# Kernel optimization log

Measured on AMD Instinct MI355X. Metric: run time of the kernel, lower is better.

Reference implementation:

```python
import jax, jax.numpy as jnp
import numpy as np

B, H, LK, D = 8, 16, 4096, 128


def setup_inputs() -> dict:
    key = jax.random.key(0)
    ks = jax.random.split(key, 9)
    s = 1.0 / np.sqrt(D)
    return {
        "Q": jax.random.normal(ks[0], (B, H, 1, D), dtype=jnp.float32),
        "K": jax.random.normal(ks[1], (B, H, LK, D), dtype=jnp.float32),
        "V": jax.random.normal(ks[2], (B, H, LK, D), dtype=jnp.float32),
        "mask": jax.random.randint(ks[3], (B, H, 1, LK), 0, 2, dtype=jnp.int32),
        "scale": 1,  # accepted but unused by the original forward
        "W_pre": jax.random.normal(ks[4], (D, D), dtype=jnp.float32) * s,
        "b_pre": jax.random.normal(ks[5], (D,), dtype=jnp.float32) * s,
        "W_q": jax.random.normal(ks[6], (D, D), dtype=jnp.float32) * s,
        "W_v": jax.random.normal(ks[7], (D, 1), dtype=jnp.float32) * s,
    }


def reference(Q, K, V, mask, scale, W_pre, b_pre, W_q, W_v):
    # precompute = linear_pre(K): [B,H,LK,D]
    pre = jnp.einsum("bhkd,de->bhke", K, W_pre) + b_pre
    # targetT = linear_q(Q): [B,H,1,D], broadcast-added over keys
    tq = jnp.einsum("bhqd,de->bhqe", Q, W_q)
    tmp = jnp.tanh(pre + tq)  # [B,H,LK,D]
    # energy = linear_v(tmp) reshaped to [B,H,1,LK]
    energy = jnp.einsum("bhkd,d->bhk", tmp, W_v[:, 0])[:, :, None, :]
    m = mask.astype(energy.dtype)
    energy = energy * (1.0 - m) + m * (-1e6)
    score = jax.nn.softmax(energy, axis=-1)  # [B,H,1,LK]
    context = jnp.matmul(score, V)  # [B,H,1,D]
    return (context, score, pre)
```

## Files before the change

kernel.cpp:

```cpp
#include <hip/hip_runtime.h>
#include <hip/hip_bf16.h>
#include <math.h>

#define B_   8
#define H_   16
#define BH_  (B_*H_)
#define LK_  4096
#define D_   128

#define SEG   16
#define KSEG  (LK_/SEG)

typedef __attribute__((ext_vector_type(8))) short bf16x8;
typedef __attribute__((ext_vector_type(4))) float f32x4;
typedef __attribute__((ext_vector_type(4))) unsigned int u32x4;

__device__ __forceinline__ float fast_tanh(float x) {
    float ax = fabsf(x);
    float e  = __expf(2.0f * ax);
    float r  = 1.0f - __fdividef(2.0f, e + 1.0f);
    return copysignf(r, x);
}

__device__ __forceinline__ unsigned int cvtpk(float lo, float hi) {
    unsigned int r;
    asm("v_cvt_pk_bf16_f32 %0, %1, %2" : "=v"(r) : "v"(lo), "v"(hi));
    return r;
}

__device__ __forceinline__ unsigned short cvt_hi(float x) {
    __hip_bfloat16 bh = __float2bfloat16(x);
    return __builtin_bit_cast(unsigned short, bh);
}

__device__ __forceinline__ void cvt8(const float4 a, const float4 b, bf16x8& h, bf16x8& l) {
    unsigned int h0 = cvtpk(a.x, a.y);
    unsigned int h1 = cvtpk(a.z, a.w);
    unsigned int h2 = cvtpk(b.x, b.y);
    unsigned int h3 = cvtpk(b.z, b.w);
    float l0 = a.x - __uint_as_float(h0 << 16);
    float l1 = a.y - __uint_as_float(h0 & 0xFFFF0000u);
    float l2 = a.z - __uint_as_float(h1 << 16);
    float l3 = a.w - __uint_as_float(h1 & 0xFFFF0000u);
    float l4 = b.x - __uint_as_float(h2 << 16);
    float l5 = b.y - __uint_as_float(h2 & 0xFFFF0000u);
    float l6 = b.z - __uint_as_float(h3 << 16);
    float l7 = b.w - __uint_as_float(h3 & 0xFFFF0000u);
    u32x4 hv = {h0, h1, h2, h3};
    u32x4 lv = {cvtpk(l0, l1), cvtpk(l2, l3), cvtpk(l4, l5), cvtpk(l6, l7)};
    h = __builtin_bit_cast(bf16x8, hv);
    l = __builtin_bit_cast(bf16x8, lv);
}

__global__ void pack_kernel(const float* __restrict__ Wpre,
                            unsigned short* __restrict__ Whi) {
    int idx  = blockIdx.x * 256 + threadIdx.x;
    int j    = idx & 7;
    int lane = (idx >> 3) & 63;
    int nt   = (idx >> 9) & 7;
    int ks   = idx >> 12;
    int k    = ks * 32 + (lane >> 4) * 8 + j;
    int n    = nt * 16 + (lane & 15);
    Whi[idx] = cvt_hi(Wpre[k * D_ + n]);
}

__global__ void tq_kernel(const float* __restrict__ Q,
                          const float* __restrict__ Wq,
                          float* __restrict__ tq) {
    int bh = blockIdx.x;
    int e  = threadIdx.x;
    const float* q = Q + bh * D_;
    float acc = 0.0f;
#pragma unroll 8
    for (int d = 0; d < D_; ++d)
        acc = fmaf(q[d], Wq[d * D_ + e], acc);
    tq[bh * D_ + e] = acc;
}

__global__ void __launch_bounds__(256, 3)
main_kernel(const float* __restrict__ K,
            const unsigned short* __restrict__ Whi,
            const float* __restrict__ bpre,
            const float* __restrict__ Wv,
            const float* __restrict__ tqg,
            float* __restrict__ pre_out,
            float* __restrict__ ep0,
            float* __restrict__ ep1) {
    const int t    = threadIdx.x;
    const int lane = t & 63;
    const int wv_  = t >> 6;
    const int kg   = wv_ & 1;
    const int eh   = wv_ >> 1;
    const int l15  = lane & 15;
    const int lg   = lane >> 4;
    const int bh   = blockIdx.y;
    const int kblk = blockIdx.x * 256;

    __shared__ unsigned short Wlds[16384];
    {
        const u32x4* src = (const u32x4*)Whi;
        u32x4* dst = (u32x4*)Wlds;
#pragma unroll
        for (int i = 0; i < 8; ++i)
            dst[i * 256 + t] = src[i * 256 + t];
    }
    __syncthreads();

    const float* Kw = K + ((size_t)bh * LK_ + kblk + kg * 32 + l15) * D_ + lg * 8;
    float* epo = (eh == 0) ? ep0 : ep1;
    const unsigned short* wb = Wlds + (size_t)(eh * 4) * 512 + (size_t)lane * 8;

    float4 rw[3][2][2];
#pragma unroll
    for (int s = 0; s < 2; ++s) {
#pragma unroll
        for (int kt = 0; kt < 2; ++kt) {
            const float* p = Kw + ((size_t)kt * 16) * D_ + s * 32;
            rw[s][kt][0] = *(const float4*)p;
            rw[s][kt][1] = *(const float4*)(p + 4);
        }
    }

#pragma unroll
    for (int it = 0; it < 4; ++it) {
        f32x4 acc[2][4];
#pragma unroll
        for (int kt = 0; kt < 2; ++kt)
#pragma unroll
            for (int et = 0; et < 4; ++et)
                acc[kt][et] = (f32x4){0.f, 0.f, 0.f, 0.f};

#pragma unroll
        for (int ks = 0; ks < 4; ++ks) {
            const int s = it * 4 + ks;
            if (s + 2 < 16) {
                const int s2  = s + 2;
                const int it2 = s2 >> 2, ks2 = s2 & 3, b2 = s2 % 3;
#pragma unroll
                for (int kt = 0; kt < 2; ++kt) {
                    const float* p = Kw + ((size_t)it2 * 64 + kt * 16) * D_ + ks2 * 32;
                    rw[b2][kt][0] = *(const float4*)p;
                    rw[b2][kt][1] = *(const float4*)(p + 4);
                }
            }
            bf16x8 wf[4];
#pragma unroll
            for (int et = 0; et < 4; ++et)
                wf[et] = *(const bf16x8*)(wb + ((size_t)ks * 8 + et) * 512);
            const int cb = s % 3;
            bf16x8 kh[2], kl[2];
            cvt8(rw[cb][0][0], rw[cb][0][1], kh[0], kl[0]);
            cvt8(rw[cb][1][0], rw[cb][1][1], kh[1], kl[1]);
#pragma unroll
            for (int kt = 0; kt < 2; ++kt)
#pragma unroll
                for (int et = 0; et < 4; ++et) {
                    acc[kt][et] = __builtin_amdgcn_mfma_f32_16x16x32_bf16(wf[et], kh[kt], acc[kt][et], 0, 0, 0);
                    acc[kt][et] = __builtin_amdgcn_mfma_f32_16x16x32_bf16(wf[et], kl[kt], acc[kt][et], 0, 0, 0);
                }
        }

        const int kb = kblk + it * 64 + kg * 32;
        float ep[2] = {0.0f, 0.0f};
#pragma unroll
        for (int et = 0; et < 4; ++et) {
            const int e0 = eh * 64 + et * 16 + lg * 4;
            const float4 bp = *(const float4*)(bpre + e0);
            const float4 tq = *(const float4*)(tqg + bh * D_ + e0);
            const float4 wv = *(const float4*)(Wv + e0);
#pragma unroll
            for (int kt = 0; kt < 2; ++kt) {
                f32x4 a = acc[kt][et];
                f32x4 v;
                v[0] = a[0] + bp.x;
                v[1] = a[1] + bp.y;
                v[2] = a[2] + bp.z;
                v[3] = a[3] + bp.w;
                float* pb = pre_out + ((size_t)bh * LK_ + kb + kt * 16 + l15) * D_ + e0;
                __builtin_nontemporal_store(v, (f32x4*)pb);
                ep[kt] = fmaf(fast_tanh(v[0] + tq.x), wv.x, ep[kt]);
                ep[kt] = fmaf(fast_tanh(v[1] + tq.y), wv.y, ep[kt]);
                ep[kt] = fmaf(fast_tanh(v[2] + tq.z), wv.z, ep[kt]);
                ep[kt] = fmaf(fast_tanh(v[3] + tq.w), wv.w, ep[kt]);
            }
        }
#pragma unroll
        for (int kt = 0; kt < 2; ++kt) {
            float v = ep[kt];
            v += __shfl_xor(v, 16, 64);
            v += __shfl_xor(v, 32, 64);
            if (lg == 0)
                epo[(size_t)bh * LK_ + kb + kt * 16 + l15] = v;
        }
    }
}

__global__ void ml_kernel(const float* __restrict__ ep0,
                          const float* __restrict__ ep1,
                          const int* __restrict__ mask,
                          float* __restrict__ ml) {
    const int bh = blockIdx.x;
    const int t  = threadIdx.x;
    const float* e0 = ep0 + (size_t)bh * LK_;
    const float* e1 = ep1 + (size_t)bh * LK_;
    const int*   m  = mask + (size_t)bh * LK_;

    float mx = -1e30f;
    for (int k = t; k < LK_; k += 256) {
        float v = m[k] ? -1.0e6f : (e0[k] + e1[k]);
        mx = fmaxf(mx, v);
    }
#pragma unroll
    for (int off = 32; off > 0; off >>= 1)
        mx = fmaxf(mx, __shfl_xor(mx, off, 64));
    __shared__ float wmax[4];
    if ((t & 63) == 0) wmax[t >> 6] = mx;
    __syncthreads();
    mx = fmaxf(fmaxf(wmax[0], wmax[1]), fmaxf(wmax[2], wmax[3]));

    float sum = 0.0f;
    for (int k = t; k < LK_; k += 256) {
        float v = m[k] ? -1.0e6f : (e0[k] + e1[k]);
        sum += __expf(v - mx);
    }
#pragma unroll
    for (int off = 32; off > 0; off >>= 1)
        sum += __shfl_xor(sum, off, 64);
    __shared__ float wsum[4];
    if ((t & 63) == 0) wsum[t >> 6] = sum;
    __syncthreads();
    if (t == 0) {
        ml[bh * 2]     = mx;
        ml[bh * 2 + 1] = wsum[0] + wsum[1] + wsum[2] + wsum[3];
    }
}

__global__ void score_ctx_kernel(const float* __restrict__ ep1,
                                 const int* __restrict__ mask,
                                 const float* __restrict__ V,
                                 const float* __restrict__ ml,
                                 float* __restrict__ score_out,
                                 float* __restrict__ part) {
    const int seg = blockIdx.x;
    const int bh  = blockIdx.y;
    const int t   = threadIdx.x;
    const int k0  = seg * KSEG;

    __shared__ float sc[KSEG];
    __shared__ float pl[8][136];

    const float mx  = ml[bh * 2];
    const float inv = 1.0f / ml[bh * 2 + 1];

    {
        const size_t gi = (size_t)bh * LK_ + k0 + t;
        float v = mask[gi] ? -1.0e6f : (score_out[gi] + ep1[gi]);
        float s = __expf(v - mx) * inv;
        sc[t] = s;
        score_out[gi] = s;
    }
    __syncthreads();

    const int d4 = t & 31;
    const int g  = t >> 5;
    const float* Vb = V + ((size_t)bh * LK_ + k0) * D_ + d4 * 4;
    float4 a = make_float4(0.f, 0.f, 0.f, 0.f);
#pragma unroll 4
    for (int kk = g; kk < KSEG; kk += 8) {
        float4 vv = *(const float4*)(Vb + (size_t)kk * D_);
        float s = sc[kk];
        a.x = fmaf(s, vv.x, a.x);
        a.y = fmaf(s, vv.y, a.y);
        a.z = fmaf(s, vv.z, a.z);
        a.w = fmaf(s, vv.w, a.w);
    }
    *(float4*)&pl[g][d4 * 4] = a;
    __syncthreads();

    if (t < 128) {
        float s = 0.0f;
#pragma unroll
        for (int gg = 0; gg < 8; ++gg)
            s += pl[gg][t];
        part[((size_t)bh * SEG + seg) * D_ + t] = s;
    }
}

__global__ void combine_kernel(const float* __restrict__ part,
                               float* __restrict__ ctx) {
    const int bh = blockIdx.x;
    const int d  = threadIdx.x;
    float s = 0.0f;
#pragma unroll
    for (int g = 0; g < SEG; ++g)
        s += part[((size_t)bh * SEG + g) * D_ + d];
    ctx[bh * D_ + d] = s;
}

extern "C" void kernel_launch(void* const* d_in, const int* in_sizes, int n_in,
                              void* d_out, int out_size, void* d_ws, size_t ws_size,
                              hipStream_t stream) {
    const float* Q    = (const float*)d_in[0];
    const float* K    = (const float*)d_in[1];
    const float* V    = (const float*)d_in[2];
    const int*   mask = (const int*)  d_in[3];
    const float* Wpre = (const float*)d_in[5];
    const float* bpre = (const float*)d_in[6];
    const float* Wq   = (const float*)d_in[7];
    const float* Wv   = (const float*)d_in[8];

    float* out   = (float*)d_out;
    float* ctx   = out;
    float* score = out + (size_t)BH_ * D_;
    float* pre   = score + (size_t)BH_ * LK_;

    float* w    = (float*)d_ws;
    float* tq   = w;
    float* ml   = tq + (size_t)BH_ * D_;
    float* part = ml + 2 * BH_;
    unsigned short* Whi = (unsigned short*)(part + (size_t)BH_ * SEG * D_);
    float* ep1  = (float*)(Whi + 16384);

    hipLaunchKernelGGL(pack_kernel, dim3(64), dim3(256), 0, stream, Wpre, Whi);
    hipLaunchKernelGGL(tq_kernel, dim3(BH_), dim3(D_), 0, stream, Q, Wq, tq);
    hipLaunchKernelGGL(main_kernel, dim3(LK_ / 256, BH_), dim3(256), 0, stream,
                       K, Whi, bpre, Wv, tq, pre, score, ep1);
    hipLaunchKernelGGL(ml_kernel, dim3(BH_), dim3(256), 0, stream, score, ep1, mask, ml);
    hipLaunchKernelGGL(score_ctx_kernel, dim3(SEG, BH_), dim3(256), 0, stream,
                       ep1, mask, V, ml, score, part);
    hipLaunchKernelGGL(combine_kernel, dim3(BH_), dim3(D_), 0, stream, part, ctx);
}
```

Measured before the change: 236.3 us.

## Stage K tiles via global_load_lds double buffering and keep W fragments in registers

Replaces direct per-thread register loads of K with asynchronous global-to-LDS loads into a double-buffered shared tile, processing 32 keys per step with a barrier after each step. The W_pre bf16 fragments are now loaded once from global memory into registers instead of being staged through LDS. The intent is to overlap K fetches with MFMA work and cut register pressure from the triple-buffered K registers. In exchange it adds a block-wide barrier every step, and the s_waitcnt vmcnt(0) also waits on the nontemporal pre_out stores, which may serialize memory traffic.

```diff
diff --git a/kernel.cpp b/kernel.cpp
--- a/kernel.cpp
+++ b/kernel.cpp
@@ -33,23 +33,30 @@
     return __builtin_bit_cast(unsigned short, bh);
 }
 
-__device__ __forceinline__ void cvt8(const float4 a, const float4 b, bf16x8& h, bf16x8& l) {
-    unsigned int h0 = cvtpk(a.x, a.y);
-    unsigned int h1 = cvtpk(a.z, a.w);
-    unsigned int h2 = cvtpk(b.x, b.y);
-    unsigned int h3 = cvtpk(b.z, b.w);
-    float l0 = a.x - __uint_as_float(h0 << 16);
-    float l1 = a.y - __uint_as_float(h0 & 0xFFFF0000u);
-    float l2 = a.z - __uint_as_float(h1 << 16);
-    float l3 = a.w - __uint_as_float(h1 & 0xFFFF0000u);
-    float l4 = b.x - __uint_as_float(h2 << 16);
-    float l5 = b.y - __uint_as_float(h2 & 0xFFFF0000u);
-    float l6 = b.z - __uint_as_float(h3 << 16);
-    float l7 = b.w - __uint_as_float(h3 & 0xFFFF0000u);
+__device__ __forceinline__ void cvt8v(const f32x4 a, const f32x4 b, bf16x8& h, bf16x8& l) {
+    unsigned int h0 = cvtpk(a[0], a[1]);
+    unsigned int h1 = cvtpk(a[2], a[3]);
+    unsigned int h2 = cvtpk(b[0], b[1]);
+    unsigned int h3 = cvtpk(b[2], b[3]);
+    float l0 = a[0] - __uint_as_float(h0 << 16);
+    float l1 = a[1] - __uint_as_float(h0 & 0xFFFF0000u);
+    float l2 = a[2] - __uint_as_float(h1 << 16);
+    float l3 = a[3] - __uint_as_float(h1 & 0xFFFF0000u);
+    float l4 = b[0] - __uint_as_float(h2 << 16);
+    float l5 = b[1] - __uint_as_float(h2 & 0xFFFF0000u);
+    float l6 = b[2] - __uint_as_float(h3 << 16);
+    float l7 = b[3] - __uint_as_float(h3 & 0xFFFF0000u);
     u32x4 hv = {h0, h1, h2, h3};
     u32x4 lv = {cvtpk(l0, l1), cvtpk(l2, l3), cvtpk(l4, l5), cvtpk(l6, l7)};
     h = __builtin_bit_cast(bf16x8, hv);
     l = __builtin_bit_cast(bf16x8, lv);
+}
+
+__device__ __forceinline__ void gld_lds16(const void* g, void* l) {
+    __builtin_amdgcn_global_load_lds(
+        (const __attribute__((address_space(1))) unsigned int*)g,
+        (__attribute__((address_space(3))) unsigned int*)l,
+        16, 0, 0);
 }
 
 __global__ void pack_kernel(const float* __restrict__ Wpre,
@@ -96,102 +103,83 @@
     const int bh   = blockIdx.y;
     const int kblk = blockIdx.x * 256;
 
-    __shared__ unsigned short Wlds[16384];
-    {
-        const u32x4* src = (const u32x4*)Whi;
-        u32x4* dst = (u32x4*)Wlds;
-#pragma unroll
-        for (int i = 0; i < 8; ++i)
-            dst[i * 256 + t] = src[i * 256 + t];
-    }
-    __syncthreads();
-
-    const float* Kw = K + ((size_t)bh * LK_ + kblk + kg * 32 + l15) * D_ + lg * 8;
-    float* epo = (eh == 0) ? ep0 : ep1;
-    const unsigned short* wb = Wlds + (size_t)(eh * 4) * 512 + (size_t)lane * 8;
-
-    float4 rw[3][2][2];
-#pragma unroll
-    for (int s = 0; s < 2; ++s) {
-#pragma unroll
-        for (int kt = 0; kt < 2; ++kt) {
-            const float* p = Kw + ((size_t)kt * 16) * D_ + s * 32;
-            rw[s][kt][0] = *(const float4*)p;
-            rw[s][kt][1] = *(const float4*)(p + 4);
+    __shared__ float Klds[2][4096];
+
+    const float* Kbh = K + (size_t)bh * LK_ * D_;
+
+    bf16x8 wf[4][4];
+#pragma unroll
+    for (int ks = 0; ks < 4; ++ks)
+#pragma unroll
+        for (int et = 0; et < 4; ++et)
+            wf[ks][et] = *(const bf16x8*)(Whi + (((size_t)ks * 8 + eh * 4 + et) * 64 + lane) * 8);
+
+    auto stageK = [&](int s, int buf) {
+#pragma unroll
+        for (int i = 0; i < 4; ++i) {
+            const int g4  = wv_ * 4 + i;
+            const int kg2 = g4 >> 3, ks2 = (g4 >> 1) & 3, h2 = g4 & 1;
+            const int row = kblk + s * 32 + kg2 * 16 + l15;
+            const int col = lg * 8 + ks2 * 32 + h2 * 4;
+            gld_lds16(Kbh + (size_t)row * D_ + col, &Klds[buf][g4 * 256]);
         }
-    }
-
-#pragma unroll
-    for (int it = 0; it < 4; ++it) {
-        f32x4 acc[2][4];
-#pragma unroll
-        for (int kt = 0; kt < 2; ++kt)
-#pragma unroll
-            for (int et = 0; et < 4; ++et)
-                acc[kt][et] = (f32x4){0.f, 0.f, 0.f, 0.f};
+    };
+
+    stageK(0, 0);
+    asm volatile("s_waitcnt vmcnt(0)\n\ts_barrier" ::: "memory");
+
+#pragma unroll
+    for (int s = 0; s < 8; ++s) {
+        if (s < 7) stageK(s + 1, (s + 1) & 1);
+
+        const float* kb = Klds[s & 1];
+        f32x4 acc[4];
+#pragma unroll
+        for (int et = 0; et < 4; ++et)
+            acc[et] = (f32x4){0.f, 0.f, 0.f, 0.f};
 
 #pragma unroll
         for (int ks = 0; ks < 4; ++ks) {
-            const int s = it * 4 + ks;
-            if (s + 2 < 16) {
-                const int s2  = s + 2;
-                const int it2 = s2 >> 2, ks2 = s2 & 3, b2 = s2 % 3;
-#pragma unroll
-                for (int kt = 0; kt < 2; ++kt) {
-                    const float* p = Kw + ((size_t)it2 * 64 + kt * 16) * D_ + ks2 * 32;
-                    rw[b2][kt][0] = *(const float4*)p;
-                    rw[b2][kt][1] = *(const float4*)(p + 4);
-                }
+            const int gbase = ((kg * 4 + ks) * 2) * 256 + lane * 4;
+            f32x4 p0 = *(const f32x4*)(kb + gbase);
+            f32x4 p1 = *(const f32x4*)(kb + gbase + 256);
+            bf16x8 kh, kl;
+            cvt8v(p0, p1, kh, kl);
+#pragma unroll
+            for (int et = 0; et < 4; ++et) {
+                acc[et] = __builtin_amdgcn_mfma_f32_16x16x32_bf16(wf[ks][et], kh, acc[et], 0, 0, 0);
+                acc[et] = __builtin_amdgcn_mfma_f32_16x16x32_bf16(wf[ks][et], kl, acc[et], 0, 0, 0);
             }
-            bf16x8 wf[4];
-#pragma unroll
-            for (int et = 0; et < 4; ++et)
-                wf[et] = *(const bf16x8*)(wb + ((size_t)ks * 8 + et) * 512);
-            const int cb = s % 3;
-            bf16x8 kh[2], kl[2];
-            cvt8(rw[cb][0][0], rw[cb][0][1], kh[0], kl[0]);
-            cvt8(rw[cb][1][0], rw[cb][1][1], kh[1], kl[1]);
-#pragma unroll
-            for (int kt = 0; kt < 2; ++kt)
-#pragma unroll
-                for (int et = 0; et < 4; ++et) {
-                    acc[kt][et] = __builtin_amdgcn_mfma_f32_16x16x32_bf16(wf[et], kh[kt], acc[kt][et], 0, 0, 0);
-                    acc[kt][et] = __builtin_amdgcn_mfma_f32_16x16x32_bf16(wf[et], kl[kt], acc[kt][et], 0, 0, 0);
-                }
         }
 
-        const int kb = kblk + it * 64 + kg * 32;
-        float ep[2] = {0.0f, 0.0f};
+        const int key = kblk + s * 32 + kg * 16 + l15;
+        float* pb = pre_out + (size_t)bh * LK_ * D_ + (size_t)key * D_;
+        float ep = 0.0f;
 #pragma unroll
         for (int et = 0; et < 4; ++et) {
             const int e0 = eh * 64 + et * 16 + lg * 4;
             const float4 bp = *(const float4*)(bpre + e0);
             const float4 tq = *(const float4*)(tqg + bh * D_ + e0);
             const float4 wv = *(const float4*)(Wv + e0);
-#pragma unroll
-            for (int kt = 0; kt < 2; ++kt) {
-                f32x4 a = acc[kt][et];
-                f32x4 v;
-                v[0] = a[0] + bp.x;
-                v[1] = a[1] + bp.y;
-                v[2] = a[2] + bp.z;
-                v[3] = a[3] + bp.w;
-                float* pb = pre_out + ((size_t)bh * LK_ + kb + kt * 16 + l15) * D_ + e0;
-                __builtin_nontemporal_store(v, (f32x4*)pb);
-                ep[kt] = fmaf(fast_tanh(v[0] + tq.x), wv.x, ep[kt]);
-                ep[kt] = fmaf(fast_tanh(v[1] + tq.y), wv.y, ep[kt]);
-                ep[kt] = fmaf(fast_tanh(v[2] + tq.z), wv.z, ep[kt]);
-                ep[kt] = fmaf(fast_tanh(v[3] + tq.w), wv.w, ep[kt]);
-            }
+            f32x4 a = acc[et];
+            f32x4 v;
+            v[0] = a[0] + bp.x;
+            v[1] = a[1] + bp.y;
+            v[2] = a[2] + bp.z;
+            v[3] = a[3] + bp.w;
+            __builtin_nontemporal_store(v, (f32x4*)(pb + e0));
+            ep = fmaf(fast_tanh(v[0] + tq.x), wv.x, ep);
+            ep = fmaf(fast_tanh(v[1] + tq.y), wv.y, ep);
+            ep = fmaf(fast_tanh(v[2] + tq.z), wv.z, ep);
+            ep = fmaf(fast_tanh(v[3] + tq.w), wv.w, ep);
         }
-#pragma unroll
-        for (int kt = 0; kt < 2; ++kt) {
-            float v = ep[kt];
-            v += __shfl_xor(v, 16, 64);
-            v += __shfl_xor(v, 32, 64);
-            if (lg == 0)
-                epo[(size_t)bh * LK_ + kb + kt * 16 + l15] = v;
+        ep += __shfl_xor(ep, 16, 64);
+        ep += __shfl_xor(ep, 32, 64);
+        if (lg == 0) {
+            float* epo = (eh == 0) ? ep0 : ep1;
+            epo[(size_t)bh * LK_ + key] = ep;
         }
+        asm volatile("s_waitcnt vmcnt(0) lgkmcnt(0)\n\ts_barrier" ::: "memory");
     }
 }
 
```

Result: no change. 237.4 us (+0.5%).
